# Performance work log

Hardware: AMD Instinct MI355X
Metric: run time of the kernel (lower is better)

## Reference

```python
import jax, jax.numpy as jnp
import numpy as np

EPS_DIST = 1e-10
BN_EPS = 1e-5
K = 3  # nsample / three_nn


def setup_inputs() -> dict:
    key = jax.random.key(0)
    ks = jax.random.split(key, 8)
    B, N, S, D1, D2 = 4, 8192, 2048, 128, 256
    C_in = D1 + D2  # 384
    H = 256
    inp = {
        "pos1": jax.random.normal(ks[0], (B, 3, N), dtype=jnp.float32),
        "pos2": jax.random.normal(ks[1], (B, 3, S), dtype=jnp.float32),
        "feature1": jax.random.normal(ks[2], (B, D1, N), dtype=jnp.float32),
        "feature2": jax.random.normal(ks[3], (B, D2, S), dtype=jnp.float32),
        # MLP layer 1: Conv1d(384->256, k=1) + BN
        "W1": jax.random.normal(ks[4], (H, C_in), dtype=jnp.float32) * (1.0 / np.sqrt(C_in)),
        "b1": jnp.zeros((H,), dtype=jnp.float32),
        "g1": jnp.ones((H,), dtype=jnp.float32),
        "be1": jnp.zeros((H,), dtype=jnp.float32),
        # MLP layer 2: Conv1d(256->256, k=1) + BN
        "W2": jax.random.normal(ks[5], (H, H), dtype=jnp.float32) * (1.0 / np.sqrt(H)),
        "b2": jnp.zeros((H,), dtype=jnp.float32),
        "g2": jnp.ones((H,), dtype=jnp.float32),
        "be2": jnp.zeros((H,), dtype=jnp.float32),
    }
    return inp


def _conv_bn_relu(x, W, b, gamma, beta):
    # x: [B, Cin, N]; 1x1 Conv1d == channel GEMM
    y = jnp.einsum("oc,bcn->bon", W, x) + b[None, :, None]
    # BatchNorm1d in training mode: batch statistics over (B, N)
    mean = jnp.mean(y, axis=(0, 2), keepdims=True)
    var = jnp.mean(jnp.square(y - mean), axis=(0, 2), keepdims=True)
    y = (y - mean) * jax.lax.rsqrt(var + BN_EPS)
    y = y * gamma[None, :, None] + beta[None, :, None]
    return jax.nn.relu(y)


def reference(pos1, pos2, feature1, feature2, W1, b1, g1, be1, W2, b2, g2, be2):
    # pos1: [B,3,N], pos2: [B,3,S], feature1: [B,D1,N], feature2: [B,D2,S]
    p1 = jnp.swapaxes(pos1, 1, 2)  # [B,N,3]
    p2 = jnp.swapaxes(pos2, 1, 2)  # [B,S,3]
    # three_nn: squared-distance 3-NN of each point in p1 among p2
    d2 = (jnp.sum(p1 * p1, -1)[:, :, None]
          + jnp.sum(p2 * p2, -1)[:, None, :]
          - 2.0 * jnp.einsum("bnc,bsc->bns", p1, p2))  # [B,N,S]
    neg_vals, idx = jax.lax.top_k(-d2, K)  # idx: [B,N,3]
    dists = jnp.maximum(-neg_vals, EPS_DIST)  # dists[dists<1e-10]=1e-10
    w = 1.0 / dists
    w = w / jnp.sum(w, -1, keepdims=True)  # [B,N,3]
    # grouping_operation: gather feature2 [B,D,S] by idx -> [B,D,N,3]
    grouped = jax.vmap(lambda f, i: f[:, i])(feature2, idx)
    interpolated = jnp.sum(grouped * w[:, None, :, :], axis=-1)  # [B,D2,N]
    feat = jnp.concatenate([interpolated, feature1], axis=1)  # [B,384,N]
    feat = _conv_bn_relu(feat, W1, b1, g1, be1)
    feat = _conv_bn_relu(feat, W2, b2, g2, be2)
    return feat  # [B,256,N]
```

## Files before the change

kernel.cpp:

```cpp
#include <hip/hip_runtime.h>
#include <hip/hip_bf16.h>
#include <cstdint>

typedef unsigned short u16;
typedef unsigned int u32;
typedef unsigned long long u64;
typedef __bf16 bf16x8 __attribute__((ext_vector_type(8)));
typedef float f32x4 __attribute__((ext_vector_type(4)));

__device__ __forceinline__ u16 f2b(float f) {
    unsigned int u = __float_as_uint(f);
    u += 0x7fffu + ((u >> 16) & 1u);
    return (u16)(u >> 16);
}
__device__ __forceinline__ float b2f(u16 h) {
    return __uint_as_float(((unsigned int)h) << 16);
}
__device__ __forceinline__ void async_cp16(void* lds, const void* g) {
    __builtin_amdgcn_global_load_lds((const __attribute__((address_space(1))) void*)g,
                                     (__attribute__((address_space(3))) void*)lds, 16, 0, 0);
}
__device__ __forceinline__ u32 fmono(float f) {
    u32 u = __float_as_uint(f);
    return u ^ (((u32)((int)u >> 31)) | 0x80000000u);
}
__device__ __forceinline__ u64 shfl_xor_u64(u64 v, int mask) {
    u32 lo = (u32)v, hi = (u32)(v >> 32);
    lo = (u32)__shfl_xor((int)lo, mask);
    hi = (u32)__shfl_xor((int)hi, mask);
    return ((u64)hi << 32) | lo;
}
__device__ __forceinline__ void ins3(u64 k, u64& k0, u64& k1, u64& k2) {
    bool c0 = k > k0, c1 = k > k1, c2 = k > k2;
    k2 = c1 ? k1 : (c2 ? k : k2);
    k1 = c0 ? k0 : (c1 ? k : k1);
    k0 = c0 ? k : k0;
}
__device__ __forceinline__ int pkix(int i) { return i + (i >> 7); }

#define NB_CVT 160
#define NB_T2  512
#define NB_T1  1024
#define NB_NN  1024

__global__ __launch_bounds__(256) void prep_kernel(const float* __restrict__ w1,
                                                   const float* __restrict__ w2,
                                                   u16* __restrict__ wb,
                                                   const float* __restrict__ feature2,
                                                   u16* __restrict__ f2t,
                                                   const float* __restrict__ feature1,
                                                   u16* __restrict__ f1t,
                                                   const float* __restrict__ pos1,
                                                   const float* __restrict__ pos2,
                                                   int* __restrict__ idx_out,
                                                   float* __restrict__ w_out) {
    __shared__ __align__(16) char smem[36096];
    int bi = blockIdx.x;
    int tid = threadIdx.x;

    if (bi < NB_CVT) {
        int i = bi * 256 + tid;
        if (i < 40960) {
            const float* src = (i < 24576) ? w1 : w2;
            int k = (i < 24576) ? i : (i - 24576);
            float4 v = *(const float4*)&src[(size_t)k * 4];
            ushort4 o;
            o.x = f2b(v.x); o.y = f2b(v.y); o.z = f2b(v.z); o.w = f2b(v.w);
            *(ushort4*)&wb[(size_t)i * 4] = o;
        }
        return;
    }
    if (bi < NB_CVT + NB_T2 + NB_T1) {
        float (*t)[65] = (float (*)[65])smem;
        const float* in; u16* out; int C, S, s0, c0, b;
        if (bi < NB_CVT + NB_T2) {
            int lin = bi - NB_CVT;
            C = 256; S = 2048; in = feature2; out = f2t;
            s0 = (lin & 31) * 64; c0 = ((lin >> 5) & 3) * 64; b = lin >> 7;
        } else {
            int lin = bi - NB_CVT - NB_T2;
            C = 128; S = 8192; in = feature1; out = f1t;
            s0 = (lin & 127) * 64; c0 = ((lin >> 7) & 1) * 64; b = lin >> 8;
        }
        const float* ib = in + (size_t)b * C * S;
        u16* ob = out + (size_t)b * S * C;
        int col = tid & 63, r0 = tid >> 6;
#pragma unroll
        for (int p = 0; p < 16; ++p) {
            int c = p * 4 + r0;
            t[c][col] = ib[(size_t)(c0 + c) * S + s0 + col];
        }
        __syncthreads();
#pragma unroll
        for (int p = 0; p < 16; ++p) {
            int s = p * 4 + r0;
            ob[(size_t)(s0 + s) * C + c0 + col] = f2b(t[col][s]);
        }
        return;
    }

    float4* pk = (float4*)smem;
    u64* warr = (u64*)(smem + 33024);
    int nb = bi - (NB_CVT + NB_T2 + NB_T1);
    int j0 = nb * 32;
    int b = j0 >> 13;
    const float* p2 = pos2 + (size_t)b * 3 * 2048;
    for (int i = tid; i < 2048; i += 256) {
        float x = p2[i], y = p2[2048 + i], z = p2[4096 + i];
        pk[pkix(i)] = make_float4(x, y, z, -0.5f * (x * x + y * y + z * z));
    }
    __syncthreads();
    int p = tid & 15, ck = tid >> 4;
    int wv = tid >> 6, lane = tid & 63;
    int na = (j0 & 8191) + p, nbq = na + 16;
    const float* p1 = pos1 + (size_t)b * 3 * 8192;
    float xa = p1[na], ya = p1[8192 + na], za = p1[16384 + na];
    float xb = p1[nbq], yb = p1[8192 + nbq], zb = p1[16384 + nbq];

    float ga0 = -3.4e38f, ga1 = -3.4e38f, ga2 = -3.4e38f;
    float gb0 = -3.4e38f, gb1 = -3.4e38f, gb2 = -3.4e38f;
    int ia0 = 0, ia1 = 0, ia2 = 0, ib0 = 0, ib1 = 0, ib2 = 0;
    int sb = ck * 128;
    const float4* pc = pk + pkix(sb);
#pragma unroll 4
    for (int it = 0; it < 128; ++it) {
        float4 cd = pc[it];
        int s = sb + it;
        float ta = fmaf(xa, cd.x, fmaf(ya, cd.y, fmaf(za, cd.z, cd.w)));
        float tb = fmaf(xb, cd.x, fmaf(yb, cd.y, fmaf(zb, cd.z, cd.w)));
        bool a0 = ta > ga0, a1 = ta > ga1, a2 = ta > ga2;
        ga2 = a1 ? ga1 : (a2 ? ta : ga2);
        ia2 = a1 ? ia1 : (a2 ? s : ia2);
        ga1 = a0 ? ga0 : (a1 ? ta : ga1);
        ia1 = a0 ? ia0 : (a1 ? s : ia1);
        ga0 = a0 ? ta : ga0;
        ia0 = a0 ? s : ia0;
        bool b0c = tb > gb0, b1c = tb > gb1, b2c = tb > gb2;
        gb2 = b1c ? gb1 : (b2c ? tb : gb2);
        ib2 = b1c ? ib1 : (b2c ? s : ib2);
        gb1 = b0c ? gb0 : (b1c ? tb : gb1);
        ib1 = b0c ? ib0 : (b1c ? s : ib1);
        gb0 = b0c ? tb : gb0;
        ib0 = b0c ? s : ib0;
    }
    u64 a0k = ((u64)fmono(ga0) << 32) | (u64)(2047 - ia0);
    u64 a1k = ((u64)fmono(ga1) << 32) | (u64)(2047 - ia1);
    u64 a2k = ((u64)fmono(ga2) << 32) | (u64)(2047 - ia2);
    u64 b0k = ((u64)fmono(gb0) << 32) | (u64)(2047 - ib0);
    u64 b1k = ((u64)fmono(gb1) << 32) | (u64)(2047 - ib1);
    u64 b2k = ((u64)fmono(gb2) << 32) | (u64)(2047 - ib2);
#pragma unroll
    for (int mask = 16; mask <= 32; mask <<= 1) {
        u64 pa0 = shfl_xor_u64(a0k, mask), pa1 = shfl_xor_u64(a1k, mask), pa2 = shfl_xor_u64(a2k, mask);
        u64 pb0 = shfl_xor_u64(b0k, mask), pb1 = shfl_xor_u64(b1k, mask), pb2 = shfl_xor_u64(b2k, mask);
        ins3(pa0, a0k, a1k, a2k); ins3(pa1, a0k, a1k, a2k); ins3(pa2, a0k, a1k, a2k);
        ins3(pb0, b0k, b1k, b2k); ins3(pb1, b0k, b1k, b2k); ins3(pb2, b0k, b1k, b2k);
    }
    if (lane < 16) {
        u64* wr = &warr[(wv * 16 + p) * 6];
        wr[0] = a0k; wr[1] = a1k; wr[2] = a2k;
        wr[3] = b0k; wr[4] = b1k; wr[5] = b2k;
    }
    __syncthreads();
    if (tid < 32) {
        int q = tid;
        int pp = q & 15, off = (q < 16) ? 0 : 3;
        const u64* w0 = &warr[pp * 6];
        u64 k0 = w0[off], k1 = w0[off + 1], k2 = w0[off + 2];
#pragma unroll
        for (int w = 1; w < 4; ++w) {
            const u64* wr = &warr[(w * 16 + pp) * 6];
            ins3(wr[off], k0, k1, k2);
            ins3(wr[off + 1], k0, k1, k2);
            ins3(wr[off + 2], k0, k1, k2);
        }
        int s0 = 2047 - (int)(k0 & 0xFFFFFFFFu);
        int s1 = 2047 - (int)(k1 & 0xFFFFFFFFu);
        int s2 = 2047 - (int)(k2 & 0xFFFFFFFFu);
        int j = j0 + q;
        int n = j & 8191;
        float x1 = p1[n], y1 = p1[8192 + n], z1 = p1[16384 + n];
        float n1 = x1 * x1 + y1 * y1 + z1 * z1;
        float4 c0v = pk[pkix(s0)], c1v = pk[pkix(s1)], c2v = pk[pkix(s2)];
        float t0 = fmaf(x1, c0v.x, fmaf(y1, c0v.y, fmaf(z1, c0v.z, c0v.w)));
        float t1 = fmaf(x1, c1v.x, fmaf(y1, c1v.y, fmaf(z1, c1v.z, c1v.w)));
        float t2 = fmaf(x1, c2v.x, fmaf(y1, c2v.y, fmaf(z1, c2v.z, c2v.w)));
        float d0 = fmaxf(fmaf(-2.f, t0, n1), 1e-10f);
        float d1 = fmaxf(fmaf(-2.f, t1, n1), 1e-10f);
        float d2 = fmaxf(fmaf(-2.f, t2, n1), 1e-10f);
        float w0v = 1.f / d0, w1v = 1.f / d1, w2v = 1.f / d2;
        float inv = 1.f / (w0v + w1v + w2v);
        idx_out[j * 3] = s0; idx_out[j * 3 + 1] = s1; idx_out[j * 3 + 2] = s2;
        w_out[j * 3] = w0v * inv; w_out[j * 3 + 1] = w1v * inv; w_out[j * 3 + 2] = w2v * inv;
    }
}

__global__ __launch_bounds__(256) void gather_kernel(const u16* __restrict__ f2t,
                                                     const int* __restrict__ idx,
                                                     const float* __restrict__ wgt,
                                                     u16* __restrict__ interp) {
    int wv = threadIdx.x >> 6, lane = threadIdx.x & 63;
    int j = blockIdx.x * 4 + wv;
    int b = j >> 13;
    int i0 = idx[j * 3], i1 = idx[j * 3 + 1], i2 = idx[j * 3 + 2];
    float w0 = wgt[j * 3], w1 = wgt[j * 3 + 1], w2 = wgt[j * 3 + 2];
    const u16* r0 = f2t + ((size_t)(b * 2048 + i0)) * 256;
    const u16* r1 = f2t + ((size_t)(b * 2048 + i1)) * 256;
    const u16* r2 = f2t + ((size_t)(b * 2048 + i2)) * 256;
    int c = lane * 4;
    ushort4 v0 = *(const ushort4*)(r0 + c);
    ushort4 v1 = *(const ushort4*)(r1 + c);
    ushort4 v2 = *(const ushort4*)(r2 + c);
    ushort4 o;
    o.x = f2b(w0 * b2f(v0.x) + w1 * b2f(v1.x) + w2 * b2f(v2.x));
    o.y = f2b(w0 * b2f(v0.y) + w1 * b2f(v1.y) + w2 * b2f(v2.y));
    o.z = f2b(w0 * b2f(v0.z) + w1 * b2f(v1.z) + w2 * b2f(v2.z));
    o.w = f2b(w0 * b2f(v0.w) + w1 * b2f(v1.w) + w2 * b2f(v2.w));
    *(ushort4*)(interp + (size_t)j * 256 + c) = o;
}

template <int KT, bool SPLIT>
__global__ __launch_bounds__(256, 2) void gemm_kernel(const u16* __restrict__ A1,
                                                      const u16* __restrict__ A2,
                                                      const u16* __restrict__ Bw,
                                                      const float* __restrict__ bias,
                                                      u16* __restrict__ Yb,
                                                      float* __restrict__ stats) {
    __shared__ u16 Al[128 * 64];
    __shared__ u16 Bl[128 * 64];
    int tid = threadIdx.x;
    int lane = tid & 63, wv = tid >> 6;
    int j0 = blockIdx.x * 128, m0 = blockIdx.y * 128;
    int l15 = lane & 15, q = lane >> 4;
    int wj = (wv >> 1) * 64, wm = (wv & 1) * 64;
    f32x4 acc[4][4];
#pragma unroll
    for (int i = 0; i < 4; ++i)
#pragma unroll
        for (int jj = 0; jj < 4; ++jj) acc[i][jj] = (f32x4){0.f, 0.f, 0.f, 0.f};

    int rbase = wv * 32;
    int lrow = lane >> 3, lchunk = lane & 7;
    const u16* Bg = Bw + (size_t)m0 * KT;

    for (int k0 = 0; k0 < KT; k0 += 64) {
        const u16* src; int stride;
        if (!SPLIT || k0 < 256) { src = A1 + (size_t)j0 * 256 + k0; stride = 256; }
        else                    { src = A2 + (size_t)j0 * 128 + (k0 - 256); stride = 128; }
#pragma unroll
        for (int qq = 0; qq < 4; ++qq) {
            int row = rbase + qq * 8;
            async_cp16(&Al[row * 64], src + (size_t)(row + lrow) * stride + lchunk * 8);
            async_cp16(&Bl[row * 64], Bg + (size_t)(row + lrow) * KT + k0 + lchunk * 8);
        }
        __syncthreads();
#pragma unroll
        for (int ks = 0; ks < 2; ++ks) {
            bf16x8 af[4], bfr[4];
#pragma unroll
            for (int i = 0; i < 4; ++i)
                af[i] = *(const bf16x8*)&Al[(wj + i * 16 + l15) * 64 + ks * 32 + q * 8];
#pragma unroll
            for (int i = 0; i < 4; ++i)
                bfr[i] = *(const bf16x8*)&Bl[(wm + i * 16 + l15) * 64 + ks * 32 + q * 8];
#pragma unroll
            for (int i = 0; i < 4; ++i)
#pragma unroll
                for (int jj = 0; jj < 4; ++jj)
                    acc[i][jj] = __builtin_amdgcn_mfma_f32_16x16x32_bf16(af[i], bfr[jj],
                                                                         acc[i][jj], 0, 0, 0);
        }
        __syncthreads();
    }
#pragma unroll
    for (int jj = 0; jj < 4; ++jj) {
        int m = m0 + wm + jj * 16 + l15;
        float bv = bias[m];
        float s = 0.f, s2 = 0.f;
#pragma unroll
        for (int i = 0; i < 4; ++i) {
            int jr = j0 + wj + i * 16 + q * 4;
#pragma unroll
            for (int r = 0; r < 4; ++r) {
                float v = acc[i][jj][r] + bv;
                s += v; s2 += v * v;
                Yb[(size_t)(jr + r) * 256 + m] = f2b(v);
            }
        }
        s += __shfl_xor(s, 16); s += __shfl_xor(s, 32);
        s2 += __shfl_xor(s2, 16); s2 += __shfl_xor(s2, 32);
        if (q == 0) {
            atomicAdd(&stats[m], s);
            atomicAdd(&stats[256 + m], s2);
        }
    }
}

__global__ __launch_bounds__(256) void apply1_kernel(const u16* __restrict__ Y1,
                                                     const float* __restrict__ stats,
                                                     const float* __restrict__ g,
                                                     const float* __restrict__ be,
                                                     u16* __restrict__ X2) {
    size_t i = ((size_t)blockIdx.x * 256 + threadIdx.x) * 4;
    int m = (int)(i & 255);
    float4 sm = *(const float4*)&stats[m];
    float4 sq = *(const float4*)&stats[256 + m];
    float4 gg = *(const float4*)&g[m];
    float4 bb = *(const float4*)&be[m];
    const float inv = 1.f / 32768.f;
    float mean, var, aa[4], ss[4];
    mean = sm.x * inv; var = sq.x * inv - mean * mean; aa[0] = gg.x * rsqrtf(var + 1e-5f); ss[0] = bb.x - mean * aa[0];
    mean = sm.y * inv; var = sq.y * inv - mean * mean; aa[1] = gg.y * rsqrtf(var + 1e-5f); ss[1] = bb.y - mean * aa[1];
    mean = sm.z * inv; var = sq.z * inv - mean * mean; aa[2] = gg.z * rsqrtf(var + 1e-5f); ss[2] = bb.z - mean * aa[2];
    mean = sm.w * inv; var = sq.w * inv - mean * mean; aa[3] = gg.w * rsqrtf(var + 1e-5f); ss[3] = bb.w - mean * aa[3];
    ushort4 v = *(const ushort4*)&Y1[i];
    ushort4 o;
    o.x = f2b(fmaxf(b2f(v.x) * aa[0] + ss[0], 0.f));
    o.y = f2b(fmaxf(b2f(v.y) * aa[1] + ss[1], 0.f));
    o.z = f2b(fmaxf(b2f(v.z) * aa[2] + ss[2], 0.f));
    o.w = f2b(fmaxf(b2f(v.w) * aa[3] + ss[3], 0.f));
    *(ushort4*)&X2[i] = o;
}

__global__ __launch_bounds__(256) void final_out_kernel(const u16* __restrict__ Y2,
                                                        const float* __restrict__ stats,
                                                        const float* __restrict__ g,
                                                        const float* __restrict__ be,
                                                        float* __restrict__ out) {
    __shared__ float t[64][65];
    int j0 = blockIdx.x * 64, o0 = blockIdx.y * 64;
    int tid = threadIdx.x;
    int c4 = (tid & 15) * 4, rw = tid >> 4;
#pragma unroll
    for (int p = 0; p < 4; ++p) {
        int jl = p * 16 + rw;
        ushort4 v = *(const ushort4*)&Y2[(size_t)(j0 + jl) * 256 + o0 + c4];
        t[jl][c4] = b2f(v.x); t[jl][c4 + 1] = b2f(v.y);
        t[jl][c4 + 2] = b2f(v.z); t[jl][c4 + 3] = b2f(v.w);
    }
    __syncthreads();
    int b = j0 >> 13, n0 = j0 & 8191;
    const float inv = 1.f / 32768.f;
#pragma unroll
    for (int p = 0; p < 4; ++p) {
        int ol = p * 16 + rw;
        int o = o0 + ol;
        float mean = stats[o] * inv;
        float var = stats[256 + o] * inv - mean * mean;
        float a = g[o] * rsqrtf(var + 1e-5f);
        float s = be[o] - mean * a;
        float4 v;
        v.x = fmaxf(t[c4][ol] * a + s, 0.f);
        v.y = fmaxf(t[c4 + 1][ol] * a + s, 0.f);
        v.z = fmaxf(t[c4 + 2][ol] * a + s, 0.f);
        v.w = fmaxf(t[c4 + 3][ol] * a + s, 0.f);
        *(float4*)&out[(size_t)b * 2097152 + (size_t)o * 8192 + n0 + c4] = v;
    }
}

extern "C" void kernel_launch(void* const* d_in, const int* in_sizes, int n_in,
                              void* d_out, int out_size, void* d_ws, size_t ws_size,
                              hipStream_t stream) {
    const float* pos1 = (const float*)d_in[0];
    const float* pos2 = (const float*)d_in[1];
    const float* feature1 = (const float*)d_in[2];
    const float* feature2 = (const float*)d_in[3];
    const float* W1 = (const float*)d_in[4];
    const float* b1 = (const float*)d_in[5];
    const float* g1 = (const float*)d_in[6];
    const float* be1 = (const float*)d_in[7];
    const float* W2 = (const float*)d_in[8];
    const float* b2 = (const float*)d_in[9];
    const float* g2 = (const float*)d_in[10];
    const float* be2 = (const float*)d_in[11];

    char* ws = (char*)d_ws;
    int*   IDX    = (int*)(ws + 0);
    float* WGT    = (float*)(ws + 393216);
    u16*   W1B    = (u16*)(ws + 786432);
    u16*   W2B    = (u16*)(ws + 983040);
    float* STATS  = (float*)(ws + 1114112);
    u16*   F2T    = (u16*)(ws + 1118208);
    u16*   F1T    = (u16*)(ws + 5312512);
    u16*   INTERP = (u16*)(ws + 13701120);
    u16*   Y1     = (u16*)(ws + 30478336);
    u16*   X2     = (u16*)(ws + 47255552);
    u16*   Y2     = (u16*)(ws + 64032768);
    float* OUT    = (float*)d_out;

    hipMemsetAsync(STATS, 0, 1024 * sizeof(float), stream);
    prep_kernel<<<NB_CVT + NB_T2 + NB_T1 + NB_NN, 256, 0, stream>>>(
        W1, W2, W1B, feature2, F2T, feature1, F1T, pos1, pos2, IDX, WGT);
    gather_kernel<<<8192, 256, 0, stream>>>(F2T, IDX, WGT, INTERP);
    gemm_kernel<384, true><<<dim3(256, 2), 256, 0, stream>>>(INTERP, F1T, W1B, b1, Y1, STATS);
    apply1_kernel<<<8192, 256, 0, stream>>>(Y1, STATS, g1, be1, X2);
    gemm_kernel<256, false><<<dim3(256, 2), 256, 0, stream>>>(X2, nullptr, W2B, b2, Y2, STATS + 512);
    final_out_kernel<<<dim3(512, 4), 256, 0, stream>>>(Y2, STATS + 512, g2, be2, OUT);
}
```

Before: 210.1 us.

## Halve 3-NN LDS footprint via two-pass staging, reorder prep blocks

The 3-NN part of the prep kernel now stages pos2 into LDS in two 1024-point halves instead of all 2048 at once, which cuts shared memory from about 36KB to about 20KB. It merges the per-half top-3 candidates into packed 64-bit keys and sets launch_bounds to target 8 blocks per CU, aiming for higher occupancy. The NN blocks are moved to the front of the grid so the heavier compute blocks start first, with the conversion and transpose blocks filling in behind. The costs are an extra barrier and LDS refill per block, plus the final distance recompute now reading pos2 from global memory.

```diff
diff --git a/kernel.cpp b/kernel.cpp
--- a/kernel.cpp
+++ b/kernel.cpp
@@ -38,47 +38,48 @@
 }
 __device__ __forceinline__ int pkix(int i) { return i + (i >> 7); }
 
+#define NB_NN  1024
 #define NB_CVT 160
 #define NB_T2  512
 #define NB_T1  1024
-#define NB_NN  1024
-
-__global__ __launch_bounds__(256) void prep_kernel(const float* __restrict__ w1,
-                                                   const float* __restrict__ w2,
-                                                   u16* __restrict__ wb,
-                                                   const float* __restrict__ feature2,
-                                                   u16* __restrict__ f2t,
-                                                   const float* __restrict__ feature1,
-                                                   u16* __restrict__ f1t,
-                                                   const float* __restrict__ pos1,
-                                                   const float* __restrict__ pos2,
-                                                   int* __restrict__ idx_out,
-                                                   float* __restrict__ w_out) {
-    __shared__ __align__(16) char smem[36096];
+
+__global__ __launch_bounds__(256, 8) void prep_kernel(const float* __restrict__ w1,
+                                                      const float* __restrict__ w2,
+                                                      u16* __restrict__ wb,
+                                                      const float* __restrict__ feature2,
+                                                      u16* __restrict__ f2t,
+                                                      const float* __restrict__ feature1,
+                                                      u16* __restrict__ f1t,
+                                                      const float* __restrict__ pos1,
+                                                      const float* __restrict__ pos2,
+                                                      int* __restrict__ idx_out,
+                                                      float* __restrict__ w_out) {
+    __shared__ __align__(16) char smem[19712];
     int bi = blockIdx.x;
     int tid = threadIdx.x;
 
-    if (bi < NB_CVT) {
-        int i = bi * 256 + tid;
-        if (i < 40960) {
-            const float* src = (i < 24576) ? w1 : w2;
-            int k = (i < 24576) ? i : (i - 24576);
-            float4 v = *(const float4*)&src[(size_t)k * 4];
-            ushort4 o;
-            o.x = f2b(v.x); o.y = f2b(v.y); o.z = f2b(v.z); o.w = f2b(v.w);
-            *(ushort4*)&wb[(size_t)i * 4] = o;
-        }
-        return;
-    }
-    if (bi < NB_CVT + NB_T2 + NB_T1) {
+    if (bi >= NB_NN) {
+        int ci = bi - NB_NN;
+        if (ci < NB_CVT) {
+            int i = ci * 256 + tid;
+            if (i < 40960) {
+                const float* src = (i < 24576) ? w1 : w2;
+                int k = (i < 24576) ? i : (i - 24576);
+                float4 v = *(const float4*)&src[(size_t)k * 4];
+                ushort4 o;
+                o.x = f2b(v.x); o.y = f2b(v.y); o.z = f2b(v.z); o.w = f2b(v.w);
+                *(ushort4*)&wb[(size_t)i * 4] = o;
+            }
+            return;
+        }
         float (*t)[65] = (float (*)[65])smem;
         const float* in; u16* out; int C, S, s0, c0, b;
-        if (bi < NB_CVT + NB_T2) {
-            int lin = bi - NB_CVT;
+        if (ci < NB_CVT + NB_T2) {
+            int lin = ci - NB_CVT;
             C = 256; S = 2048; in = feature2; out = f2t;
             s0 = (lin & 31) * 64; c0 = ((lin >> 5) & 3) * 64; b = lin >> 7;
         } else {
-            int lin = bi - NB_CVT - NB_T2;
+            int lin = ci - NB_CVT - NB_T2;
             C = 128; S = 8192; in = feature1; out = f1t;
             s0 = (lin & 127) * 64; c0 = ((lin >> 7) & 1) * 64; b = lin >> 8;
         }
@@ -100,16 +101,10 @@
     }
 
     float4* pk = (float4*)smem;
-    u64* warr = (u64*)(smem + 33024);
-    int nb = bi - (NB_CVT + NB_T2 + NB_T1);
-    int j0 = nb * 32;
+    u64* warr = (u64*)(smem + 16512);
+    int j0 = bi * 32;
     int b = j0 >> 13;
     const float* p2 = pos2 + (size_t)b * 3 * 2048;
-    for (int i = tid; i < 2048; i += 256) {
-        float x = p2[i], y = p2[2048 + i], z = p2[4096 + i];
-        pk[pkix(i)] = make_float4(x, y, z, -0.5f * (x * x + y * y + z * z));
-    }
-    __syncthreads();
     int p = tid & 15, ck = tid >> 4;
     int wv = tid >> 6, lane = tid & 63;
     int na = (j0 & 8191) + p, nbq = na + 16;
@@ -117,38 +112,55 @@
     float xa = p1[na], ya = p1[8192 + na], za = p1[16384 + na];
     float xb = p1[nbq], yb = p1[8192 + nbq], zb = p1[16384 + nbq];
 
-    float ga0 = -3.4e38f, ga1 = -3.4e38f, ga2 = -3.4e38f;
-    float gb0 = -3.4e38f, gb1 = -3.4e38f, gb2 = -3.4e38f;
-    int ia0 = 0, ia1 = 0, ia2 = 0, ib0 = 0, ib1 = 0, ib2 = 0;
-    int sb = ck * 128;
-    const float4* pc = pk + pkix(sb);
+    u64 a0k = 0, a1k = 0, a2k = 0, b0k = 0, b1k = 0, b2k = 0;
+
+    for (int half = 0; half < 2; ++half) {
+        int hbase = half * 1024;
+        for (int i = tid; i < 1024; i += 256) {
+            int s = hbase + i;
+            float x = p2[s], y = p2[2048 + s], z = p2[4096 + s];
+            pk[pkix(i)] = make_float4(x, y, z, -0.5f * (x * x + y * y + z * z));
+        }
+        __syncthreads();
+
+        float ga0 = -3.4e38f, ga1 = -3.4e38f, ga2 = -3.4e38f;
+        float gb0 = -3.4e38f, gb1 = -3.4e38f, gb2 = -3.4e38f;
+        int ia0 = 0, ia1 = 0, ia2 = 0, ib0 = 0, ib1 = 0, ib2 = 0;
+        int sb = ck * 64;
+        const float4* pc = pk + pkix(sb);
 #pragma unroll 4
-    for (int it = 0; it < 128; ++it) {
-        float4 cd = pc[it];
-        int s = sb + it;
-        float ta = fmaf(xa, cd.x, fmaf(ya, cd.y, fmaf(za, cd.z, cd.w)));
-        float tb = fmaf(xb, cd.x, fmaf(yb, cd.y, fmaf(zb, cd.z, cd.w)));
-        bool a0 = ta > ga0, a1 = ta > ga1, a2 = ta > ga2;
-        ga2 = a1 ? ga1 : (a2 ? ta : ga2);
-        ia2 = a1 ? ia1 : (a2 ? s : ia2);
-        ga1 = a0 ? ga0 : (a1 ? ta : ga1);
-        ia1 = a0 ? ia0 : (a1 ? s : ia1);
-        ga0 = a0 ? ta : ga0;
-        ia0 = a0 ? s : ia0;
-        bool b0c = tb > gb0, b1c = tb > gb1, b2c = tb > gb2;
-        gb2 = b1c ? gb1 : (b2c ? tb : gb2);
-        ib2 = b1c ? ib1 : (b2c ? s : ib2);
-        gb1 = b0c ? gb0 : (b1c ? tb : gb1);
-        ib1 = b0c ? ib0 : (b1c ? s : ib1);
-        gb0 = b0c ? tb : gb0;
-        ib0 = b0c ? s : ib0;
-    }
-    u64 a0k = ((u64)fmono(ga0) << 32) | (u64)(2047 - ia0);
-    u64 a1k = ((u64)fmono(ga1) << 32) | (u64)(2047 - ia1);
-    u64 a2k = ((u64)fmono(ga2) << 32) | (u64)(2047 - ia2);
-    u64 b0k = ((u64)fmono(gb0) << 32) | (u64)(2047 - ib0);
-    u64 b1k = ((u64)fmono(gb1) << 32) | (u64)(2047 - ib1);
-    u64 b2k = ((u64)fmono(gb2) << 32) | (u64)(2047 - ib2);
+        for (int it = 0; it < 64; ++it) {
+            float4 cd = pc[it];
+            int s = sb + it;
+            float ta = fmaf(xa, cd.x, fmaf(ya, cd.y, fmaf(za, cd.z, cd.w)));
+            float tb = fmaf(xb, cd.x, fmaf(yb, cd.y, fmaf(zb, cd.z, cd.w)));
+            bool a0 = ta > ga0, a1 = ta > ga1, a2 = ta > ga2;
+            ga2 = a1 ? ga1 : (a2 ? ta : ga2);
+            ia2 = a1 ? ia1 : (a2 ? s : ia2);
+            ga1 = a0 ? ga0 : (a1 ? ta : ga1);
+            ia1 = a0 ? ia0 : (a1 ? s : ia1);
+            ga0 = a0 ? ta : ga0;
+            ia0 = a0 ? s : ia0;
+            bool b0c = tb > gb0, b1c = tb > gb1, b2c = tb > gb2;
+            gb2 = b1c ? gb1 : (b2c ? tb : gb2);
+            ib2 = b1c ? ib1 : (b2c ? s : ib2);
+            gb1 = b0c ? gb0 : (b1c ? tb : gb1);
+            ib1 = b0c ? ib0 : (b1c ? s : ib1);
+            gb0 = b0c ? tb : gb0;
+            ib0 = b0c ? s : ib0;
+        }
+        __syncthreads();
+
+        int gi0 = hbase + ia0, gi1 = hbase + ia1, gi2 = hbase + ia2;
+        int gj0 = hbase + ib0, gj1 = hbase + ib1, gj2 = hbase + ib2;
+        ins3(((u64)fmono(ga0) << 32) | (u64)(2047 - gi0), a0k, a1k, a2k);
+        ins3(((u64)fmono(ga1) << 32) | (u64)(2047 - gi1), a0k, a1k, a2k);
+        ins3(((u64)fmono(ga2) << 32) | (u64)(2047 - gi2), a0k, a1k, a2k);
+        ins3(((u64)fmono(gb0) << 32) | (u64)(2047 - gj0), b0k, b1k, b2k);
+        ins3(((u64)fmono(gb1) << 32) | (u64)(2047 - gj1), b0k, b1k, b2k);
+        ins3(((u64)fmono(gb2) << 32) | (u64)(2047 - gj2), b0k, b1k, b2k);
+    }
+
 #pragma unroll
     for (int mask = 16; mask <= 32; mask <<= 1) {
         u64 pa0 = shfl_xor_u64(a0k, mask), pa1 = shfl_xor_u64(a1k, mask), pa2 = shfl_xor_u64(a2k, mask);
@@ -181,10 +193,12 @@
         int n = j & 8191;
         float x1 = p1[n], y1 = p1[8192 + n], z1 = p1[16384 + n];
         float n1 = x1 * x1 + y1 * y1 + z1 * z1;
-        float4 c0v = pk[pkix(s0)], c1v = pk[pkix(s1)], c2v = pk[pkix(s2)];
-        float t0 = fmaf(x1, c0v.x, fmaf(y1, c0v.y, fmaf(z1, c0v.z, c0v.w)));
-        float t1 = fmaf(x1, c1v.x, fmaf(y1, c1v.y, fmaf(z1, c1v.z, c1v.w)));
-        float t2 = fmaf(x1, c2v.x, fmaf(y1, c2v.y, fmaf(z1, c2v.z, c2v.w)));
+        float X0 = p2[s0], Y0 = p2[2048 + s0], Z0 = p2[4096 + s0];
+        float X1 = p2[s1], Y1v = p2[2048 + s1], Z1 = p2[4096 + s1];
+        float X2 = p2[s2], Y2v = p2[2048 + s2], Z2 = p2[4096 + s2];
+        float t0 = x1 * X0 + y1 * Y0 + z1 * Z0 - 0.5f * (X0 * X0 + Y0 * Y0 + Z0 * Z0);
+        float t1 = x1 * X1 + y1 * Y1v + z1 * Z1 - 0.5f * (X1 * X1 + Y1v * Y1v + Z1 * Z1);
+        float t2 = x1 * X2 + y1 * Y2v + z1 * Z2 - 0.5f * (X2 * X2 + Y2v * Y2v + Z2 * Z2);
         float d0 = fmaxf(fmaf(-2.f, t0, n1), 1e-10f);
         float d1 = fmaxf(fmaf(-2.f, t1, n1), 1e-10f);
         float d2 = fmaxf(fmaf(-2.f, t2, n1), 1e-10f);
@@ -389,7 +403,7 @@
     float* OUT    = (float*)d_out;
 
     hipMemsetAsync(STATS, 0, 1024 * sizeof(float), stream);
-    prep_kernel<<<NB_CVT + NB_T2 + NB_T1 + NB_NN, 256, 0, stream>>>(
+    prep_kernel<<<NB_NN + NB_CVT + NB_T2 + NB_T1, 256, 0, stream>>>(
         W1, W2, W1B, feature2, F2T, feature1, F1T, pos1, pos2, IDX, WGT);
     gather_kernel<<<8192, 256, 0, stream>>>(F2T, IDX, WGT, INTERP);
     gemm_kernel<384, true><<<dim3(256, 2), 256, 0, stream>>>(INTERP, F1T, W1B, b1, Y1, STATS);
```

New measurement: 209.0 us. Within noise of the previous version (-0.5%).
